# Kernel tuning notes

Measured on AMD Instinct MI355X. Metric: run time of the kernel, lower is better.

Reference implementation:

```python
import jax, jax.numpy as jnp
import numpy as np

B, N, H, E, A, V, L = 64, 196, 512, 512, 512, 20000, 20


def setup_inputs() -> dict:
    key = jax.random.key(0)
    ks = jax.random.split(key, 16)
    s = lambda *sh: 0.02
    return {
        "encoder_outputs": jax.random.normal(ks[0], (B, N, H), dtype=jnp.float32),
        "captions": jax.random.randint(ks[1], (B, L), 0, V, dtype=jnp.int64),
        "emb": jax.random.normal(ks[2], (V, E), dtype=jnp.float32) * 0.02,
        "W_ih": jax.random.normal(ks[3], (4 * H, E + H), dtype=jnp.float32) * 0.02,
        "W_hh": jax.random.normal(ks[4], (4 * H, H), dtype=jnp.float32) * 0.02,
        "b_ih": jax.random.normal(ks[5], (4 * H,), dtype=jnp.float32) * 0.02,
        "b_hh": jax.random.normal(ks[6], (4 * H,), dtype=jnp.float32) * 0.02,
        "enc_W": jax.random.normal(ks[7], (A, H), dtype=jnp.float32) * 0.02,
        "enc_b": jax.random.normal(ks[8], (A,), dtype=jnp.float32) * 0.02,
        "dec_W": jax.random.normal(ks[9], (A, H), dtype=jnp.float32) * 0.02,
        "dec_b": jax.random.normal(ks[10], (A,), dtype=jnp.float32) * 0.02,
        "energy_W": jax.random.normal(ks[11], (1, A), dtype=jnp.float32) * 0.02,
        "energy_b": jax.random.normal(ks[12], (1,), dtype=jnp.float32) * 0.02,
        "fc_W": jax.random.normal(ks[13], (V, H), dtype=jnp.float32) * 0.02,
        "fc_b": jax.random.normal(ks[14], (V,), dtype=jnp.float32) * 0.02,
    }


def reference(encoder_outputs, captions, emb, W_ih, W_hh, b_ih, b_hh,
              enc_W, enc_b, dec_W, dec_b, energy_W, energy_b, fc_W, fc_b):
    b, max_len = captions.shape
    hid = W_hh.shape[1]
    vocab = fc_W.shape[0]
    dt = encoder_outputs.dtype

    # encoder projection is hidden-state independent: hoist out of the loop
    enc_proj = jnp.einsum('bnh,ah->bna', encoder_outputs, enc_W) + enc_b  # [B,N,A]
    # teacher forcing ratio = 1.0 => input at step t is captions[:, t-1]
    emb_seq = emb[captions[:, :-1]]                                      # [B,L-1,E]
    emb_seq = jnp.swapaxes(emb_seq, 0, 1)                                # [L-1,B,E]

    def step(carry, x_t):
        h, c = carry
        dec = h @ dec_W.T + dec_b                                        # [B,A]
        scores = jnp.tanh(enc_proj + dec[:, None, :]) @ energy_W[0] + energy_b[0]  # [B,N]
        attw = jax.nn.softmax(scores, axis=1)
        context = jnp.einsum('bn,bnh->bh', attw, encoder_outputs)        # [B,H]
        lstm_in = jnp.concatenate([x_t, context], axis=1)                # [B,E+H]
        gates = lstm_in @ W_ih.T + b_ih + h @ W_hh.T + b_hh              # [B,4H]
        i, f, g, o = jnp.split(gates, 4, axis=1)
        c_new = jax.nn.sigmoid(f) * c + jax.nn.sigmoid(i) * jnp.tanh(g)
        h_new = jax.nn.sigmoid(o) * jnp.tanh(c_new)
        out = h_new @ fc_W.T + fc_b                                      # [B,V]
        return (h_new, c_new), out

    h0 = jnp.zeros((b, hid), dtype=dt)
    c0 = jnp.zeros((b, hid), dtype=dt)
    (_, _), outs = jax.lax.scan(step, (h0, c0), emb_seq)                 # [L-1,B,V]
    outputs = jnp.concatenate(
        [jnp.zeros((b, 1, vocab), dtype=dt), jnp.swapaxes(outs, 0, 1)], axis=1)
    return outputs
```

## Files before the change

kernel.cpp:

```cpp
#include <hip/hip_runtime.h>
#include <hip/hip_bf16.h>
#include <math.h>

#define B   64
#define NN  196
#define HH  512
#define EE  512
#define AA  512
#define VV  20000
#define LL  20

#define TM 64
#define TN 64
#define TK 16

typedef __attribute__((ext_vector_type(8))) short bf16x8;
typedef __attribute__((ext_vector_type(4))) float floatx4;

__device__ __forceinline__ float tanh_fast(float x) {
  float e2 = __expf(2.f * x);
  return 1.f - 2.f / (e2 + 1.f);
}
__device__ __forceinline__ float sigmoid_fast(float x) {
  return 1.f / (1.f + __expf(-x));
}
__device__ __forceinline__ float bf2f(unsigned short u) {
  return __uint_as_float(((unsigned)u) << 16);
}
__device__ __forceinline__ unsigned short f2bf(float v) {
  __hip_bfloat16 h = __float2bfloat16(v);
  return *reinterpret_cast<unsigned short*>(&h);
}

__global__ __launch_bounds__(256) void gemm_mfma_bt(
    const unsigned short* __restrict__ Xb, const unsigned short* __restrict__ Wb,
    const float* __restrict__ bias, float* __restrict__ C,
    int M, int N, int K, int ldC, int outMode, int gridMX) {
  __shared__ unsigned short As[128 * 32];
  __shared__ unsigned short Bs[128 * 32];
  const int tid = threadIdx.x;
  const int lane = tid & 63;
  const int l15 = lane & 15;
  const int q = lane >> 4;
  const int wv = tid >> 6;
  const int wm = (wv >> 1) * 64;
  const int wn = (wv & 1) * 64;
  const int mBase = (gridMX ? blockIdx.x : blockIdx.y) * 128;
  const int nBase = (gridMX ? blockIdx.y : blockIdx.x) * 128;

  const int c0 = tid, c1 = tid + 256;
  const int r0 = c0 >> 2, o0 = (c0 & 3) * 8;
  const int r1 = c1 >> 2, o1 = (c1 & 3) * 8;

  floatx4 zero = {0.f, 0.f, 0.f, 0.f};
  floatx4 acc[4][4];
#pragma unroll
  for (int i = 0; i < 4; ++i)
#pragma unroll
    for (int j = 0; j < 4; ++j) acc[i][j] = zero;

  for (int k0 = 0; k0 < K; k0 += 32) {
    uint4 a0 = *(const uint4*)(Xb + (size_t)(mBase + r0) * K + k0 + o0);
    uint4 a1 = *(const uint4*)(Xb + (size_t)(mBase + r1) * K + k0 + o1);
    uint4 b0 = *(const uint4*)(Wb + (size_t)(nBase + r0) * K + k0 + o0);
    uint4 b1 = *(const uint4*)(Wb + (size_t)(nBase + r1) * K + k0 + o1);
    __syncthreads();
    *(uint4*)&As[c0 * 8] = a0;
    *(uint4*)&As[c1 * 8] = a1;
    *(uint4*)&Bs[c0 * 8] = b0;
    *(uint4*)&Bs[c1 * 8] = b1;
    __syncthreads();
    bf16x8 af[4], bfv[4];
#pragma unroll
    for (int i = 0; i < 4; ++i)
      af[i] = *(const bf16x8*)&As[(wm + i * 16 + l15) * 32 + q * 8];
#pragma unroll
    for (int j = 0; j < 4; ++j)
      bfv[j] = *(const bf16x8*)&Bs[(wn + j * 16 + l15) * 32 + q * 8];
#pragma unroll
    for (int i = 0; i < 4; ++i)
#pragma unroll
      for (int j = 0; j < 4; ++j)
        acc[i][j] = __builtin_amdgcn_mfma_f32_16x16x32_bf16(af[i], bfv[j],
                                                            acc[i][j], 0, 0, 0);
  }

#pragma unroll
  for (int i = 0; i < 4; ++i) {
#pragma unroll
    for (int j = 0; j < 4; ++j) {
#pragma unroll
      for (int p = 0; p < 4; ++p) {
        int m = mBase + wm + i * 16 + q * 4 + p;
        int n = nBase + wn + j * 16 + l15;
        if (m < M && n < N) {
          float v = acc[i][j][p];
          if (bias) v += bias[n];
          if (outMode == 1) {
            size_t idx = (size_t)(m & 63) * ((size_t)LL * VV) +
                         (size_t)((m >> 6) + 1) * VV + n;
            C[idx] = v;
          } else if (outMode == 2) {
            ((unsigned short*)C)[(size_t)m * ldC + n] = f2bf(v);
          } else {
            C[(size_t)m * ldC + n] = v;
          }
        }
      }
    }
  }
}

__global__ __launch_bounds__(256) void convert_pad(
    const float* __restrict__ src, unsigned short* __restrict__ dst,
    int srcRows, int dstRows, int srcStride, int colOff) {
  int idx = blockIdx.x * 256 + threadIdx.x;
  if (idx >= dstRows * 512) return;
  int r = idx >> 9, cc = idx & 511;
  float v = (r < srcRows) ? src[(size_t)r * srcStride + colOff + cc] : 0.f;
  dst[idx] = f2bf(v);
}

__global__ __launch_bounds__(256) void gemm_skinny(
    const float* __restrict__ X, const float* __restrict__ W,
    float* __restrict__ part, int K, int Ks) {
  __shared__ float Xs[TK][TM + 4];
  __shared__ float Ws[TK][TN + 4];
  const int nBase = blockIdx.x * TN;
  const int kBase = blockIdx.y * Ks;
  const int tid = threadIdx.x;
  const int tx = tid & 15;
  const int ty = tid >> 4;
  float acc[4][4] = {};

  for (int k0 = kBase; k0 < kBase + Ks; k0 += TK) {
#pragma unroll
    for (int i = 0; i < 4; ++i) {
      int e = tid + i * 256;
      int r = e >> 4;
      int cc = e & 15;
      Xs[cc][r] = X[(size_t)r * K + k0 + cc];
      Ws[cc][r] = W[(size_t)(nBase + r) * K + k0 + cc];
    }
    __syncthreads();
#pragma unroll
    for (int kk = 0; kk < TK; ++kk) {
      float xv[4], wvv[4];
#pragma unroll
      for (int i = 0; i < 4; ++i) xv[i] = Xs[kk][ty * 4 + i];
#pragma unroll
      for (int j = 0; j < 4; ++j) wvv[j] = Ws[kk][tx * 4 + j];
#pragma unroll
      for (int i = 0; i < 4; ++i)
#pragma unroll
        for (int j = 0; j < 4; ++j) acc[i][j] += xv[i] * wvv[j];
    }
    __syncthreads();
  }

  float* o = part + (size_t)blockIdx.y * (64 * 2048);
#pragma unroll
  for (int i = 0; i < 4; ++i) {
    int m = ty * 4 + i;
    float4 r4;
    r4.x = acc[i][0]; r4.y = acc[i][1]; r4.z = acc[i][2]; r4.w = acc[i][3];
    *(float4*)(o + (size_t)m * 2048 + nBase + tx * 4) = r4;
  }
}

__global__ __launch_bounds__(256) void build_weights(
    const float* __restrict__ W_ih, const float* __restrict__ W_hh,
    const float* __restrict__ b_ih, const float* __restrict__ b_hh,
    float* __restrict__ Wb3, float* __restrict__ bsum) {
  int idx = blockIdx.x * 256 + threadIdx.x;
  if (idx < 2048 * 1024) {
    int n = idx >> 10, k = idx & 1023;
    Wb3[idx] = (k < 512) ? W_hh[(size_t)n * 512 + k]
                         : W_ih[(size_t)n * 1024 + 512 + (k - 512)];
  }
  if (idx < 2048) bsum[idx] = b_ih[idx] + b_hh[idx];
}

__global__ __launch_bounds__(256) void gather_emb(
    const float* __restrict__ emb, const int* __restrict__ captions,
    unsigned short* __restrict__ embx) {
  int m = blockIdx.x;
  int tid = threadIdx.x;
  if (m >= 1216) {
    embx[(size_t)m * 512 + tid] = 0;
    embx[(size_t)m * 512 + 256 + tid] = 0;
    return;
  }
  int t = m >> 6, b = m & 63;
  int cap = captions[b * LL + t];
#pragma unroll
  for (int i = 0; i < 2; ++i) {
    float v = emb[(size_t)cap * 512 + i * 256 + tid];
    embx[(size_t)m * 512 + i * 256 + tid] = f2bf(v);
  }
}

__global__ __launch_bounds__(256) void zero_t0_kernel(float* __restrict__ out) {
  int idx = blockIdx.x * 256 + threadIdx.x;
  if (idx < B * VV) {
    int b = idx / VV, v = idx % VV;
    out[(size_t)b * ((size_t)LL * VV) + v] = 0.f;
  }
}

__global__ __launch_bounds__(256) void lstm_pointwise2(
    const float* __restrict__ gates_base, const float* __restrict__ gates_part,
    float* __restrict__ c, float* __restrict__ xcat,
    unsigned short* __restrict__ hbt, unsigned short* __restrict__ hb_row,
    int isFirst) {
  int idx = blockIdx.x * 256 + threadIdx.x;
  int b = idx >> 9, j = idx & 511;
  float hn;
  if (isFirst) {
    hn = 0.f;
  } else {
    const float* gb = gates_base + (size_t)b * 2048;
    const float* gp = gates_part + (size_t)b * 2048;
    float ig = gb[j], fg = gb[512 + j], gg = gb[1024 + j], og = gb[1536 + j];
#pragma unroll
    for (int s = 0; s < 8; ++s) {
      const float* p = gp + (size_t)s * (64 * 2048);
      ig += p[j];
      fg += p[512 + j];
      gg += p[1024 + j];
      og += p[1536 + j];
    }
    float cn = sigmoid_fast(fg) * c[idx] + sigmoid_fast(ig) * tanh_fast(gg);
    hn = sigmoid_fast(og) * tanh_fast(cn);
    c[idx] = cn;
    hb_row[idx] = f2bf(hn);
  }
  hbt[idx] = f2bf(hn);
  xcat[(size_t)b * 1024 + j] = hn;
}

__global__ __launch_bounds__(512) void attn_score_ctx(
    const unsigned short* __restrict__ enc_projb,
    const unsigned short* __restrict__ encOutb,
    const float* __restrict__ dec_buf, const float* __restrict__ eW,
    const float* __restrict__ eb, float* __restrict__ xcat) {
  int b = blockIdx.x;
  int tid = threadIdx.x;
  __shared__ float sw[NN];
  __shared__ float tmp[256];
  __shared__ float cp[1024];

  int wvv = tid >> 6, lane = tid & 63;
  float ew8[8], sd8[8];
  const float* db = dec_buf + (size_t)b * 512;
#pragma unroll
  for (int j = 0; j < 8; ++j) {
    ew8[j] = eW[lane * 8 + j];
    sd8[j] = db[lane * 8 + j];
  }
  float eb0 = eb[0];
  for (int n = wvv; n < NN; n += 8) {
    const unsigned short* ep = enc_projb + ((size_t)b * NN + n) * 512 + lane * 8;
    bf16x8 v8 = *(const bf16x8*)ep;
    float a = 0.f;
#pragma unroll
    for (int j = 0; j < 8; ++j)
      a += tanh_fast(bf2f((unsigned short)v8[j]) + sd8[j]) * ew8[j];
#pragma unroll
    for (int off = 32; off; off >>= 1) a += __shfl_down(a, off, 64);
    if (lane == 0) sw[n] = a + eb0;
  }
  __syncthreads();

  float v = (tid < NN) ? sw[tid] : -1e30f;
  if (tid < 256) tmp[tid] = v;
  __syncthreads();
  for (int s = 128; s; s >>= 1) {
    if (tid < s) tmp[tid] = fmaxf(tmp[tid], tmp[tid + s]);
    __syncthreads();
  }
  float mx = tmp[0];
  __syncthreads();
  float e = (tid < NN) ? __expf(v - mx) : 0.f;
  if (tid < 256) tmp[tid] = e;
  __syncthreads();
  for (int s = 128; s; s >>= 1) {
    if (tid < s) tmp[tid] += tmp[tid + s];
    __syncthreads();
  }
  float inv = 1.f / tmp[0];
  if (tid < NN) sw[tid] = e * inv;
  __syncthreads();

  int half = tid >> 8, hp = tid & 255;
  const unsigned short* eo = encOutb + (size_t)b * NN * 512 + hp * 2;
  float a0 = 0.f, a1 = 0.f;
  int n0 = half * 98;
#pragma unroll 7
  for (int n = n0; n < n0 + 98; ++n) {
    float w = sw[n];
    unsigned u = *(const unsigned*)(eo + (size_t)n * 512);
    a0 += w * __uint_as_float((u & 0xffffu) << 16);
    a1 += w * __uint_as_float((u >> 16) << 16);
  }
  cp[half * 512 + hp * 2] = a0;
  cp[half * 512 + hp * 2 + 1] = a1;
  __syncthreads();
  xcat[(size_t)b * 1024 + 512 + tid] = cp[tid] + cp[512 + tid];
}

__global__ __launch_bounds__(256) void final_h(
    const float* __restrict__ gates_base, const float* __restrict__ gates_part,
    const float* __restrict__ c, unsigned short* __restrict__ hb19) {
  int idx = blockIdx.x * 256 + threadIdx.x;
  int b = idx >> 9, j = idx & 511;
  const float* gb = gates_base + (size_t)b * 2048;
  const float* gp = gates_part + (size_t)b * 2048;
  float ig = gb[j], fg = gb[512 + j], gg = gb[1024 + j], og = gb[1536 + j];
#pragma unroll
  for (int s = 0; s < 8; ++s) {
    const float* p = gp + (size_t)s * (64 * 2048);
    ig += p[j];
    fg += p[512 + j];
    gg += p[1024 + j];
    og += p[1536 + j];
  }
  float cn = sigmoid_fast(fg) * c[idx] + sigmoid_fast(ig) * tanh_fast(gg);
  float hn = sigmoid_fast(og) * tanh_fast(cn);
  hb19[idx] = f2bf(hn);
}

extern "C" void kernel_launch(void* const* d_in, const int* in_sizes, int n_in,
                              void* d_out, int out_size, void* d_ws, size_t ws_size,
                              hipStream_t stream) {
  const float* enc_out  = (const float*)d_in[0];
  const int*   captions = (const int*)d_in[1];
  const float* emb      = (const float*)d_in[2];
  const float* W_ih     = (const float*)d_in[3];
  const float* W_hh     = (const float*)d_in[4];
  const float* b_ih     = (const float*)d_in[5];
  const float* b_hh     = (const float*)d_in[6];
  const float* enc_W    = (const float*)d_in[7];
  const float* enc_b    = (const float*)d_in[8];
  const float* dec_W    = (const float*)d_in[9];
  const float* dec_b    = (const float*)d_in[10];
  const float* energy_W = (const float*)d_in[11];
  const float* energy_b = (const float*)d_in[12];
  const float* fc_W     = (const float*)d_in[13];
  const float* fc_b     = (const float*)d_in[14];
  float* out = (float*)d_out;

  float* ws = (float*)d_ws;
  float* c          = ws;
  float* xcat       = c + 32768;
  float* dec_buf    = xcat + 65536;
  float* gates_all  = dec_buf + 32768;
  float* gates_part = gates_all + (size_t)19 * 131072;
  float* Wb3        = gates_part + (size_t)8 * 131072;
  float* bsum       = Wb3 + (size_t)2048 * 1024;
  unsigned short* enc_projb = (unsigned short*)(bsum + 2048);
  unsigned short* fcWb    = enc_projb + (size_t)12544 * 512;
  unsigned short* encWb   = fcWb + (size_t)20096 * 512;
  unsigned short* encOutb = encWb + (size_t)512 * 512;
  unsigned short* Wb0b    = encOutb + (size_t)12544 * 512;
  unsigned short* dec_Wb  = Wb0b + (size_t)2048 * 512;
  unsigned short* embxb   = dec_Wb + (size_t)512 * 512;
  unsigned short* hb      = embxb + (size_t)1280 * 512;
  unsigned short* hbt     = hb + (size_t)1280 * 512;

  hipMemsetAsync(c, 0, 32768 * sizeof(float), stream);
  hipMemsetAsync(hb + (size_t)1216 * 512, 0,
                 (size_t)64 * 512 * sizeof(unsigned short), stream);
  zero_t0_kernel<<<(B * VV + 255) / 256, 256, 0, stream>>>(out);

  build_weights<<<(2048 * 1024) / 256, 256, 0, stream>>>(
      W_ih, W_hh, b_ih, b_hh, Wb3, bsum);

  convert_pad<<<(20096 * 512) / 256, 256, 0, stream>>>(fc_W, fcWb, 20000, 20096, 512, 0);
  convert_pad<<<(512 * 512) / 256, 256, 0, stream>>>(enc_W, encWb, 512, 512, 512, 0);
  convert_pad<<<(12544 * 512) / 256, 256, 0, stream>>>(enc_out, encOutb, 12544, 12544, 512, 0);
  convert_pad<<<(2048 * 512) / 256, 256, 0, stream>>>(W_ih, Wb0b, 2048, 2048, 1024, 0);
  convert_pad<<<(512 * 512) / 256, 256, 0, stream>>>(dec_W, dec_Wb, 512, 512, 512, 0);

  gather_emb<<<1280, 256, 0, stream>>>(emb, captions, embxb);

  gemm_mfma_bt<<<dim3(16, 10), 256, 0, stream>>>(
      embxb, Wb0b, bsum, gates_all, 1216, 2048, 512, 2048, 0, 0);

  gemm_mfma_bt<<<dim3(4, 98), 256, 0, stream>>>(
      encOutb, encWb, enc_b, (float*)enc_projb, 12544, 512, 512, 512, 2, 0);

  for (int s = 0; s < LL - 1; ++s) {
    lstm_pointwise2<<<(B * HH) / 256, 256, 0, stream>>>(
        s ? (gates_all + (size_t)(s - 1) * 131072) : nullptr, gates_part, c,
        xcat, hbt, hb + (size_t)(s > 0 ? s - 1 : 0) * 32768, s == 0 ? 1 : 0);

    gemm_mfma_bt<<<dim3(4, 1), 256, 0, stream>>>(
        hbt, dec_Wb, dec_b, dec_buf, 64, 512, 512, 512, 0, 0);

    attn_score_ctx<<<B, 512, 0, stream>>>(enc_projb, encOutb, dec_buf,
                                          energy_W, energy_b, xcat);

    gemm_skinny<<<dim3(2048 / TN, 8), 256, 0, stream>>>(xcat, Wb3, gates_part,
                                                        1024, 128);
  }

  final_h<<<(B * HH) / 256, 256, 0, stream>>>(
      gates_all + (size_t)18 * 131072, gates_part, c, hb + (size_t)1152 * 512);

  gemm_mfma_bt<<<dim3(10, 157), 256, 0, stream>>>(
      hb, fcWb, fc_b, out, 1216, 20000, 512, 0, 1, 1);
}
```

Measured before the change: 1.594 ms.

## Fuse LSTM pointwise into a joint h-projection GEMM and use MFMA for gates

Each step's LSTM pointwise update now happens inside a new kernel that keeps h in swizzled LDS and multiplies it by a concatenated [dec_W; W_hh] bf16 weight, producing both the attention decoder projection and the recurrent gate contribution in one launch. The fp32 split-K skinny GEMM over the [h, ctx] concat is replaced by an MFMA bf16 GEMM over the context only, whose epilogue adds the recurrent and embedding gate terms. This drops the partial-sum reduction and one launch per step. It also pads the LDS tiles to cut bank conflicts and remaps the final vocab GEMM grid to group tiles by XCD. The trade-offs are bf16 rounding of the context and recurrent weights, and each of the 20 gemm_h blocks redundantly recomputing the pointwise update.

Measured after the change: 2.436 ms. +52.8%, slower.

```diff
diff --git a/kernel.cpp b/kernel.cpp
--- a/kernel.cpp
+++ b/kernel.cpp
@@ -10,9 +10,7 @@
 #define VV  20000
 #define LL  20
 
-#define TM 64
-#define TN 64
-#define TK 16
+#define LDT 40
 
 typedef __attribute__((ext_vector_type(8))) short bf16x8;
 typedef __attribute__((ext_vector_type(4))) float floatx4;
@@ -35,9 +33,10 @@
 __global__ __launch_bounds__(256) void gemm_mfma_bt(
     const unsigned short* __restrict__ Xb, const unsigned short* __restrict__ Wb,
     const float* __restrict__ bias, float* __restrict__ C,
-    int M, int N, int K, int ldC, int outMode, int gridMX) {
-  __shared__ unsigned short As[128 * 32];
-  __shared__ unsigned short Bs[128 * 32];
+    int M, int N, int K, int ldC, int outMode, int gridMX,
+    const float* __restrict__ add1, const float* __restrict__ add2) {
+  __shared__ unsigned short As[128 * LDT];
+  __shared__ unsigned short Bs[128 * LDT];
   const int tid = threadIdx.x;
   const int lane = tid & 63;
   const int l15 = lane & 15;
@@ -45,8 +44,20 @@
   const int wv = tid >> 6;
   const int wm = (wv >> 1) * 64;
   const int wn = (wv & 1) * 64;
-  const int mBase = (gridMX ? blockIdx.x : blockIdx.y) * 128;
-  const int nBase = (gridMX ? blockIdx.y : blockIdx.x) * 128;
+  int mBase, nBase;
+  if (gridMX == 2) {
+    const int MT = (M + 127) >> 7, NT = (N + 127) >> 7;
+    int wg = blockIdx.x;
+    int xcd = wg & 7, idx = wg >> 3;
+    int kk = idx / MT, mi = idx - kk * MT;
+    int p = kk * 8 + xcd;
+    if (p >= NT) return;
+    mBase = mi * 128;
+    nBase = p * 128;
+  } else {
+    mBase = blockIdx.y * 128;
+    nBase = blockIdx.x * 128;
+  }
 
   const int c0 = tid, c1 = tid + 256;
   const int r0 = c0 >> 2, o0 = (c0 & 3) * 8;
@@ -65,18 +76,18 @@
     uint4 b0 = *(const uint4*)(Wb + (size_t)(nBase + r0) * K + k0 + o0);
     uint4 b1 = *(const uint4*)(Wb + (size_t)(nBase + r1) * K + k0 + o1);
     __syncthreads();
-    *(uint4*)&As[c0 * 8] = a0;
-    *(uint4*)&As[c1 * 8] = a1;
-    *(uint4*)&Bs[c0 * 8] = b0;
-    *(uint4*)&Bs[c1 * 8] = b1;
+    *(uint4*)&As[r0 * LDT + o0] = a0;
+    *(uint4*)&As[r1 * LDT + o1] = a1;
+    *(uint4*)&Bs[r0 * LDT + o0] = b0;
+    *(uint4*)&Bs[r1 * LDT + o1] = b1;
     __syncthreads();
     bf16x8 af[4], bfv[4];
 #pragma unroll
     for (int i = 0; i < 4; ++i)
-      af[i] = *(const bf16x8*)&As[(wm + i * 16 + l15) * 32 + q * 8];
+      af[i] = *(const bf16x8*)&As[(wm + i * 16 + l15) * LDT + q * 8];
 #pragma unroll
     for (int j = 0; j < 4; ++j)
-      bfv[j] = *(const bf16x8*)&Bs[(wn + j * 16 + l15) * 32 + q * 8];
+      bfv[j] = *(const bf16x8*)&Bs[(wn + j * 16 + l15) * LDT + q * 8];
 #pragma unroll
     for (int i = 0; i < 4; ++i)
 #pragma unroll
@@ -102,10 +113,106 @@
             C[idx] = v;
           } else if (outMode == 2) {
             ((unsigned short*)C)[(size_t)m * ldC + n] = f2bf(v);
+          } else if (outMode == 4) {
+            C[(size_t)m * 2048 + n] =
+                v + add1[(size_t)m * 2560 + 512 + n] + add2[(size_t)m * 2048 + n];
           } else {
             C[(size_t)m * ldC + n] = v;
           }
         }
+      }
+    }
+  }
+}
+
+__global__ __launch_bounds__(256) void gemm_h(
+    const float* __restrict__ gt,
+    const float* __restrict__ c_old,
+    float* __restrict__ c_new,
+    unsigned short* __restrict__ hb_row,
+    const unsigned short* __restrict__ Wcatb,
+    float* __restrict__ hgd,
+    int isFirst) {
+  __shared__ unsigned short hsL[64 * 512];
+  __shared__ unsigned short Bs[128 * LDT];
+  const int tid = threadIdx.x;
+  const int lane = tid & 63;
+  const int l15 = lane & 15;
+  const int q = lane >> 4;
+  const int wv = tid >> 6;
+  const int wn = wv * 32;
+  const int nBase = blockIdx.x * 128;
+
+  if (isFirst) {
+    for (int e = tid; e < 16384; e += 256) ((unsigned*)hsL)[e] = 0u;
+  } else {
+#pragma unroll 4
+    for (int it = 0; it < 64; ++it) {
+      int e2 = (it * 256 + tid) * 2;
+      int b = e2 >> 9, j = e2 & 511;
+      const float* g = gt + (size_t)b * 2048 + j;
+      float2 gi = *(const float2*)(g);
+      float2 gf = *(const float2*)(g + 512);
+      float2 gg = *(const float2*)(g + 1024);
+      float2 go = *(const float2*)(g + 1536);
+      float2 cc = *(const float2*)(c_old + e2);
+      float cn0 = sigmoid_fast(gf.x) * cc.x + sigmoid_fast(gi.x) * tanh_fast(gg.x);
+      float cn1 = sigmoid_fast(gf.y) * cc.y + sigmoid_fast(gi.y) * tanh_fast(gg.y);
+      float hn0 = sigmoid_fast(go.x) * tanh_fast(cn0);
+      float hn1 = sigmoid_fast(go.y) * tanh_fast(cn1);
+      if (blockIdx.x == 0) {
+        *(float2*)(c_new + e2) = make_float2(cn0, cn1);
+        unsigned hp = (unsigned)f2bf(hn0) | ((unsigned)f2bf(hn1) << 16);
+        *(unsigned*)&hb_row[e2] = hp;
+      }
+      unsigned hp2 = (unsigned)f2bf(hn0) | ((unsigned)f2bf(hn1) << 16);
+      *(unsigned*)&hsL[b * 512 + (j ^ ((b & 7) << 3))] = hp2;
+    }
+  }
+
+  const int c0 = tid, c1 = tid + 256;
+  const int r0 = c0 >> 2, o0 = (c0 & 3) * 8;
+  const int r1 = c1 >> 2, o1 = (c1 & 3) * 8;
+  const int rs = (l15 & 7) << 3;
+
+  floatx4 zero = {0.f, 0.f, 0.f, 0.f};
+  floatx4 acc[4][2];
+#pragma unroll
+  for (int i = 0; i < 4; ++i)
+#pragma unroll
+    for (int j = 0; j < 2; ++j) acc[i][j] = zero;
+
+  for (int k0 = 0; k0 < 512; k0 += 32) {
+    uint4 b0 = *(const uint4*)(Wcatb + (size_t)(nBase + r0) * 512 + k0 + o0);
+    uint4 b1 = *(const uint4*)(Wcatb + (size_t)(nBase + r1) * 512 + k0 + o1);
+    __syncthreads();
+    *(uint4*)&Bs[r0 * LDT + o0] = b0;
+    *(uint4*)&Bs[r1 * LDT + o1] = b1;
+    __syncthreads();
+    bf16x8 af[4], bfv[2];
+#pragma unroll
+    for (int i = 0; i < 4; ++i)
+      af[i] = *(const bf16x8*)&hsL[(i * 16 + l15) * 512 + ((k0 + q * 8) ^ rs)];
+#pragma unroll
+    for (int j = 0; j < 2; ++j)
+      bfv[j] = *(const bf16x8*)&Bs[(wn + j * 16 + l15) * LDT + q * 8];
+#pragma unroll
+    for (int i = 0; i < 4; ++i)
+#pragma unroll
+      for (int j = 0; j < 2; ++j)
+        acc[i][j] = __builtin_amdgcn_mfma_f32_16x16x32_bf16(af[i], bfv[j],
+                                                            acc[i][j], 0, 0, 0);
+  }
+
+#pragma unroll
+  for (int i = 0; i < 4; ++i) {
+#pragma unroll
+    for (int j = 0; j < 2; ++j) {
+#pragma unroll
+      for (int p = 0; p < 4; ++p) {
+        int m = i * 16 + q * 4 + p;
+        int n = nBase + wn + j * 16 + l15;
+        hgd[(size_t)m * 2560 + n] = acc[i][j][p];
       }
     }
   }
@@ -121,63 +228,10 @@
   dst[idx] = f2bf(v);
 }
 
-__global__ __launch_bounds__(256) void gemm_skinny(
-    const float* __restrict__ X, const float* __restrict__ W,
-    float* __restrict__ part, int K, int Ks) {
-  __shared__ float Xs[TK][TM + 4];
-  __shared__ float Ws[TK][TN + 4];
-  const int nBase = blockIdx.x * TN;
-  const int kBase = blockIdx.y * Ks;
-  const int tid = threadIdx.x;
-  const int tx = tid & 15;
-  const int ty = tid >> 4;
-  float acc[4][4] = {};
-
-  for (int k0 = kBase; k0 < kBase + Ks; k0 += TK) {
-#pragma unroll
-    for (int i = 0; i < 4; ++i) {
-      int e = tid + i * 256;
-      int r = e >> 4;
-      int cc = e & 15;
-      Xs[cc][r] = X[(size_t)r * K + k0 + cc];
-      Ws[cc][r] = W[(size_t)(nBase + r) * K + k0 + cc];
-    }
-    __syncthreads();
-#pragma unroll
-    for (int kk = 0; kk < TK; ++kk) {
-      float xv[4], wvv[4];
-#pragma unroll
-      for (int i = 0; i < 4; ++i) xv[i] = Xs[kk][ty * 4 + i];
-#pragma unroll
-      for (int j = 0; j < 4; ++j) wvv[j] = Ws[kk][tx * 4 + j];
-#pragma unroll
-      for (int i = 0; i < 4; ++i)
-#pragma unroll
-        for (int j = 0; j < 4; ++j) acc[i][j] += xv[i] * wvv[j];
-    }
-    __syncthreads();
-  }
-
-  float* o = part + (size_t)blockIdx.y * (64 * 2048);
-#pragma unroll
-  for (int i = 0; i < 4; ++i) {
-    int m = ty * 4 + i;
-    float4 r4;
-    r4.x = acc[i][0]; r4.y = acc[i][1]; r4.z = acc[i][2]; r4.w = acc[i][3];
-    *(float4*)(o + (size_t)m * 2048 + nBase + tx * 4) = r4;
-  }
-}
-
-__global__ __launch_bounds__(256) void build_weights(
-    const float* __restrict__ W_ih, const float* __restrict__ W_hh,
+__global__ __launch_bounds__(256) void bsum_kernel(
     const float* __restrict__ b_ih, const float* __restrict__ b_hh,
-    float* __restrict__ Wb3, float* __restrict__ bsum) {
+    float* __restrict__ bsum) {
   int idx = blockIdx.x * 256 + threadIdx.x;
-  if (idx < 2048 * 1024) {
-    int n = idx >> 10, k = idx & 1023;
-    Wb3[idx] = (k < 512) ? W_hh[(size_t)n * 512 + k]
-                         : W_ih[(size_t)n * 1024 + 512 + (k - 512)];
-  }
   if (idx < 2048) bsum[idx] = b_ih[idx] + b_hh[idx];
 }
 
@@ -208,42 +262,12 @@
   }
 }
 
-__global__ __launch_bounds__(256) void lstm_pointwise2(
-    const float* __restrict__ gates_base, const float* __restrict__ gates_part,
-    float* __restrict__ c, float* __restrict__ xcat,
-    unsigned short* __restrict__ hbt, unsigned short* __restrict__ hb_row,
-    int isFirst) {
-  int idx = blockIdx.x * 256 + threadIdx.x;
-  int b = idx >> 9, j = idx & 511;
-  float hn;
-  if (isFirst) {
-    hn = 0.f;
-  } else {
-    const float* gb = gates_base + (size_t)b * 2048;
-    const float* gp = gates_part + (size_t)b * 2048;
-    float ig = gb[j], fg = gb[512 + j], gg = gb[1024 + j], og = gb[1536 + j];
-#pragma unroll
-    for (int s = 0; s < 8; ++s) {
-      const float* p = gp + (size_t)s * (64 * 2048);
-      ig += p[j];
-      fg += p[512 + j];
-      gg += p[1024 + j];
-      og += p[1536 + j];
-    }
-    float cn = sigmoid_fast(fg) * c[idx] + sigmoid_fast(ig) * tanh_fast(gg);
-    hn = sigmoid_fast(og) * tanh_fast(cn);
-    c[idx] = cn;
-    hb_row[idx] = f2bf(hn);
-  }
-  hbt[idx] = f2bf(hn);
-  xcat[(size_t)b * 1024 + j] = hn;
-}
-
 __global__ __launch_bounds__(512) void attn_score_ctx(
     const unsigned short* __restrict__ enc_projb,
     const unsigned short* __restrict__ encOutb,
-    const float* __restrict__ dec_buf, const float* __restrict__ eW,
-    const float* __restrict__ eb, float* __restrict__ xcat) {
+    const float* __restrict__ hgd, const float* __restrict__ dec_b,
+    const float* __restrict__ eW, const float* __restrict__ eb,
+    unsigned short* __restrict__ ctxb) {
   int b = blockIdx.x;
   int tid = threadIdx.x;
   __shared__ float sw[NN];
@@ -252,11 +276,11 @@
 
   int wvv = tid >> 6, lane = tid & 63;
   float ew8[8], sd8[8];
-  const float* db = dec_buf + (size_t)b * 512;
+  const float* db = hgd + (size_t)b * 2560;
 #pragma unroll
   for (int j = 0; j < 8; ++j) {
     ew8[j] = eW[lane * 8 + j];
-    sd8[j] = db[lane * 8 + j];
+    sd8[j] = db[lane * 8 + j] + dec_b[lane * 8 + j];
   }
   float eb0 = eb[0];
   for (int n = wvv; n < NN; n += 8) {
@@ -306,26 +330,17 @@
   cp[half * 512 + hp * 2] = a0;
   cp[half * 512 + hp * 2 + 1] = a1;
   __syncthreads();
-  xcat[(size_t)b * 1024 + 512 + tid] = cp[tid] + cp[512 + tid];
+  ctxb[(size_t)b * 512 + tid] = f2bf(cp[tid] + cp[512 + tid]);
 }
 
 __global__ __launch_bounds__(256) void final_h(
-    const float* __restrict__ gates_base, const float* __restrict__ gates_part,
-    const float* __restrict__ c, unsigned short* __restrict__ hb19) {
+    const float* __restrict__ gt, const float* __restrict__ c_old,
+    unsigned short* __restrict__ hb19) {
   int idx = blockIdx.x * 256 + threadIdx.x;
   int b = idx >> 9, j = idx & 511;
-  const float* gb = gates_base + (size_t)b * 2048;
-  const float* gp = gates_part + (size_t)b * 2048;
-  float ig = gb[j], fg = gb[512 + j], gg = gb[1024 + j], og = gb[1536 + j];
-#pragma unroll
-  for (int s = 0; s < 8; ++s) {
-    const float* p = gp + (size_t)s * (64 * 2048);
-    ig += p[j];
-    fg += p[512 + j];
-    gg += p[1024 + j];
-    og += p[1536 + j];
-  }
-  float cn = sigmoid_fast(fg) * c[idx] + sigmoid_fast(ig) * tanh_fast(gg);
+  const float* g = gt + (size_t)b * 2048;
+  float ig = g[j], fg = g[512 + j], gg = g[1024 + j], og = g[1536 + j];
+  float cn = sigmoid_fast(fg) * c_old[idx] + sigmoid_fast(ig) * tanh_fast(gg);
   float hn = sigmoid_fast(og) * tanh_fast(cn);
   hb19[idx] = f2bf(hn);
 }
@@ -351,63 +366,68 @@
   float* out = (float*)d_out;
 
   float* ws = (float*)d_ws;
-  float* c          = ws;
-  float* xcat       = c + 32768;
-  float* dec_buf    = xcat + 65536;
-  float* gates_all  = dec_buf + 32768;
-  float* gates_part = gates_all + (size_t)19 * 131072;
-  float* Wb3        = gates_part + (size_t)8 * 131072;
-  float* bsum       = Wb3 + (size_t)2048 * 1024;
+  float* c2          = ws;
+  float* gates_all   = c2 + 2 * 32768;
+  float* gates_total = gates_all + (size_t)19 * 131072;
+  float* hgd         = gates_total + 131072;
+  float* bsum        = hgd + 2 * 163840;
   unsigned short* enc_projb = (unsigned short*)(bsum + 2048);
   unsigned short* fcWb    = enc_projb + (size_t)12544 * 512;
   unsigned short* encWb   = fcWb + (size_t)20096 * 512;
   unsigned short* encOutb = encWb + (size_t)512 * 512;
   unsigned short* Wb0b    = encOutb + (size_t)12544 * 512;
-  unsigned short* dec_Wb  = Wb0b + (size_t)2048 * 512;
-  unsigned short* embxb   = dec_Wb + (size_t)512 * 512;
+  unsigned short* Wicb    = Wb0b + (size_t)2048 * 512;
+  unsigned short* Wcatb   = Wicb + (size_t)2048 * 512;
+  unsigned short* embxb   = Wcatb + (size_t)2560 * 512;
   unsigned short* hb      = embxb + (size_t)1280 * 512;
-  unsigned short* hbt     = hb + (size_t)1280 * 512;
-
-  hipMemsetAsync(c, 0, 32768 * sizeof(float), stream);
+  unsigned short* ctxb    = hb + (size_t)1280 * 512;
+
+  hipMemsetAsync(c2, 0, 32768 * sizeof(float), stream);
   hipMemsetAsync(hb + (size_t)1216 * 512, 0,
                  (size_t)64 * 512 * sizeof(unsigned short), stream);
+  hipMemsetAsync(ctxb + (size_t)64 * 512, 0,
+                 (size_t)64 * 512 * sizeof(unsigned short), stream);
   zero_t0_kernel<<<(B * VV + 255) / 256, 256, 0, stream>>>(out);
 
-  build_weights<<<(2048 * 1024) / 256, 256, 0, stream>>>(
-      W_ih, W_hh, b_ih, b_hh, Wb3, bsum);
+  bsum_kernel<<<8, 256, 0, stream>>>(b_ih, b_hh, bsum);
 
   convert_pad<<<(20096 * 512) / 256, 256, 0, stream>>>(fc_W, fcWb, 20000, 20096, 512, 0);
   convert_pad<<<(512 * 512) / 256, 256, 0, stream>>>(enc_W, encWb, 512, 512, 512, 0);
   convert_pad<<<(12544 * 512) / 256, 256, 0, stream>>>(enc_out, encOutb, 12544, 12544, 512, 0);
   convert_pad<<<(2048 * 512) / 256, 256, 0, stream>>>(W_ih, Wb0b, 2048, 2048, 1024, 0);
-  convert_pad<<<(512 * 512) / 256, 256, 0, stream>>>(dec_W, dec_Wb, 512, 512, 512, 0);
+  convert_pad<<<(2048 * 512) / 256, 256, 0, stream>>>(W_ih, Wicb, 2048, 2048, 1024, 512);
+  convert_pad<<<(512 * 512) / 256, 256, 0, stream>>>(dec_W, Wcatb, 512, 512, 512, 0);
+  convert_pad<<<(2048 * 512) / 256, 256, 0, stream>>>(W_hh, Wcatb + (size_t)512 * 512,
+                                                      2048, 2048, 512, 0);
 
   gather_emb<<<1280, 256, 0, stream>>>(emb, captions, embxb);
 
   gemm_mfma_bt<<<dim3(16, 10), 256, 0, stream>>>(
-      embxb, Wb0b, bsum, gates_all, 1216, 2048, 512, 2048, 0, 0);
+      embxb, Wb0b, bsum, gates_all, 1216, 2048, 512, 2048, 0, 0, nullptr, nullptr);
 
   gemm_mfma_bt<<<dim3(4, 98), 256, 0, stream>>>(
-      encOutb, encWb, enc_b, (float*)enc_projb, 12544, 512, 512, 512, 2, 0);
+      encOutb, encWb, enc_b, (float*)enc_projb, 12544, 512, 512, 512, 2, 0,
+      nullptr, nullptr);
 
   for (int s = 0; s < LL - 1; ++s) {
-    lstm_pointwise2<<<(B * HH) / 256, 256, 0, stream>>>(
-        s ? (gates_all + (size_t)(s - 1) * 131072) : nullptr, gates_part, c,
-        xcat, hbt, hb + (size_t)(s > 0 ? s - 1 : 0) * 32768, s == 0 ? 1 : 0);
-
-    gemm_mfma_bt<<<dim3(4, 1), 256, 0, stream>>>(
-        hbt, dec_Wb, dec_b, dec_buf, 64, 512, 512, 512, 0, 0);
-
-    attn_score_ctx<<<B, 512, 0, stream>>>(enc_projb, encOutb, dec_buf,
-                                          energy_W, energy_b, xcat);
-
-    gemm_skinny<<<dim3(2048 / TN, 8), 256, 0, stream>>>(xcat, Wb3, gates_part,
-                                                        1024, 128);
-  }
-
-  final_h<<<(B * HH) / 256, 256, 0, stream>>>(
-      gates_all + (size_t)18 * 131072, gates_part, c, hb + (size_t)1152 * 512);
-
-  gemm_mfma_bt<<<dim3(10, 157), 256, 0, stream>>>(
-      hb, fcWb, fc_b, out, 1216, 20000, 512, 0, 1, 1);
-}
+    float* hgd_cur = hgd + (size_t)(s & 1) * 163840;
+    gemm_h<<<20, 256, 0, stream>>>(
+        gates_total, c2 + (size_t)((s + 1) & 1) * 32768,
+        c2 + (size_t)(s & 1) * 32768,
+        s ? hb + (size_t)(s - 1) * 32768 : nullptr, Wcatb, hgd_cur,
+        s == 0 ? 1 : 0);
+
+    attn_score_ctx<<<B, 512, 0, stream>>>(enc_projb, encOutb, hgd_cur, dec_b,
+                                          energy_W, energy_b, ctxb);
+
+    gemm_mfma_bt<<<dim3(16, 1), 256, 0, stream>>>(
+        ctxb, Wicb, nullptr, gates_total, 64, 2048, 512, 2048, 4, 0, hgd_cur,
+        gates_all + (size_t)s * 131072);
+  }
+
+  final_h<<<(B * HH) / 256, 256, 0, stream>>>(gates_total, c2,
+                                              hb + (size_t)1152 * 512);
+
+  gemm_mfma_bt<<<1600, 256, 0, stream>>>(
+      hb, fcWb, fc_b, out, 1216, 20000, 512, 0, 1, 2, nullptr, nullptr);
+}
```
